# Optimization experiments

Hardware: AMD Instinct MI355X
Metric: run time of the kernel (lower is better)

## Reference

```python
import jax, jax.numpy as jnp
import numpy as np

N_DRUGS = 4096; N_GENE = 5414; N_KG = N_DRUGS + N_GENE
N_MOL = 131072; E_MOL = 524288; E_KG = 524288; R = 8
MLP_IN = 1024; MLP_H = 512; D = 256; GCN_IN = 64; GCN_H = 128
DIM1 = 256; DIM2 = 128; DIM3 = 64; NCLS = 2
EPS = 1e-5


def setup_inputs() -> dict:
    key = jax.random.key(0)
    ks = jax.random.split(key, 32)
    def n(i, shape, fan):
        return jax.random.normal(ks[i], shape, dtype=jnp.float32) * (1.0 / np.sqrt(fan))
    inp = {}
    inp['fp_data'] = jax.random.normal(ks[0], (N_DRUGS, MLP_IN), dtype=jnp.float32)
    inp['mol_x'] = jax.random.normal(ks[1], (N_MOL, GCN_IN), dtype=jnp.float32)
    inp['mol_batch'] = jnp.sort(jax.random.randint(ks[2], (N_MOL,), 0, N_DRUGS))
    inp['mol_edge_index'] = jax.random.randint(ks[3], (2, E_MOL), 0, N_MOL)
    inp['kg_edge_index'] = jax.random.randint(ks[4], (2, E_KG), 0, N_KG)
    inp['kg_edge_type'] = jax.random.randint(ks[5], (E_KG,), 0, R)
    # parameters
    inp['fp_w1'] = n(6, (MLP_IN, MLP_H), MLP_IN); inp['fp_b1'] = jnp.zeros((MLP_H,), jnp.float32)
    inp['fp_w2'] = n(7, (MLP_H, D), MLP_H);       inp['fp_b2'] = jnp.zeros((D,), jnp.float32)
    inp['gcn_w1'] = n(8, (GCN_IN, GCN_H), GCN_IN); inp['gcn_b1'] = jnp.zeros((GCN_H,), jnp.float32)
    inp['gcn_w2'] = n(9, (GCN_H, D), GCN_H);       inp['gcn_b2'] = jnp.zeros((D,), jnp.float32)
    inp['att_w1'] = n(10, (D, 128), D); inp['att_b1'] = jnp.zeros((128,), jnp.float32)
    inp['att_w2'] = n(11, (128,), 128)
    inp['gene_emb'] = jax.random.normal(ks[12], (N_GENE, D), dtype=jnp.float32)
    inp['rg_w1'] = n(13, (R, D, DIM1), D); inp['rg_root1'] = n(14, (D, DIM1), D); inp['rg_b1'] = jnp.zeros((DIM1,), jnp.float32)
    inp['rg_w2'] = n(15, (R, DIM1, DIM2), DIM1); inp['rg_root2'] = n(16, (DIM1, DIM2), DIM1); inp['rg_b2'] = jnp.zeros((DIM2,), jnp.float32)
    inp['lin1_w'] = n(17, (DIM2, DIM3), DIM2); inp['lin1_b'] = jnp.zeros((DIM3,), jnp.float32)
    inp['lin2_w'] = n(18, (DIM3, NCLS), DIM3); inp['lin2_b'] = jnp.zeros((NCLS,), jnp.float32)
    return inp


def bn(x):
    # BatchNorm1d with batch statistics (gamma=1, beta=0)
    m = jnp.mean(x, axis=0, keepdims=True)
    v = jnp.var(x, axis=0, keepdims=True)
    return (x - m) * jax.lax.rsqrt(v + EPS)


def gcn_conv(x, w, b, src, dst, num_nodes):
    # PyG GCNConv: self-loops + symmetric normalization
    loop = jnp.arange(num_nodes, dtype=src.dtype)
    src = jnp.concatenate([src, loop]); dst = jnp.concatenate([dst, loop])
    h = x @ w  # [N, F]
    deg = jnp.zeros((num_nodes,), x.dtype).at[dst].add(1.0)
    dinv = jax.lax.rsqrt(jnp.maximum(deg, 1.0))
    norm = dinv[src] * dinv[dst]  # [E]
    out = jnp.zeros_like(h).at[dst].add(h[src] * norm[:, None])
    return out + b


def rgcn_conv(x, w, root, b, src, dst, etype, num_nodes):
    # PyG RGCNConv (aggr='mean' per relation): out_i = x_i @ root + b + sum_r mean_{j in N_r(i)} x_j @ W_r
    h = jnp.einsum('nd,rdf->rnf', x, w)          # [R, N, F]
    msg = h[etype, src]                          # [E, F] gather by (relation, source)
    cnt = jnp.zeros((R, num_nodes), x.dtype).at[etype, dst].add(1.0)
    norm = 1.0 / jnp.maximum(cnt[etype, dst], 1.0)  # [E]
    agg = jnp.zeros((num_nodes, w.shape[-1]), x.dtype).at[dst].add(msg * norm[:, None])
    return agg + x @ root + b


def forward(fp_data, mol_x, mol_batch, mol_edge_index, kg_edge_index, kg_edge_type,
            fp_w1, fp_b1, fp_w2, fp_b2, gcn_w1, gcn_b1, gcn_w2, gcn_b2,
            att_w1, att_b1, att_w2, gene_emb,
            rg_w1, rg_root1, rg_b1, rg_w2, rg_root2, rg_b2,
            lin1_w, lin1_b, lin2_w, lin2_b):
    # fingerprint MLP branch
    fp = jax.nn.relu(bn(fp_data @ fp_w1 + fp_b1))
    fp = jax.nn.relu(bn(fp @ fp_w2 + fp_b2))      # [N_DRUGS, D]
    # molecular GCN branch (batched graph replaces the dataloader loop)
    msrc, mdst = mol_edge_index[0], mol_edge_index[1]
    g = jax.nn.relu(bn(gcn_conv(mol_x, gcn_w1, gcn_b1, msrc, mdst, N_MOL)))
    g = jax.nn.relu(bn(gcn_conv(g, gcn_w2, gcn_b2, msrc, mdst, N_MOL)))  # [N_MOL, D]
    # global mean pool per molecule
    gsum = jnp.zeros((N_DRUGS, D), g.dtype).at[mol_batch].add(g)
    gcnt = jnp.zeros((N_DRUGS,), g.dtype).at[mol_batch].add(1.0)
    graph_out = gsum / jnp.maximum(gcnt, 1.0)[:, None]  # [N_DRUGS, D]
    # attention fusion of the two views
    z = jnp.stack([graph_out, fp], axis=1)        # [N_DRUGS, 2, D]
    w = jnp.tanh(z @ att_w1 + att_b1) @ att_w2    # [N_DRUGS, 2]
    beta = jax.nn.softmax(w, axis=1)
    emb = jnp.sum(beta[:, :, None] * z, axis=1)   # [N_DRUGS, D]
    # knowledge graph RGCN over drugs + genes
    x = jnp.concatenate([emb, gene_emb], axis=0)  # [N_KG, D]
    ksrc, kdst = kg_edge_index[0], kg_edge_index[1]
    x = jax.nn.relu(bn(rgcn_conv(x, rg_w1, rg_root1, rg_b1, ksrc, kdst, kg_edge_type, N_KG)))
    x = jax.nn.relu(bn(rgcn_conv(x, rg_w2, rg_root2, rg_b2, ksrc, kdst, kg_edge_type, N_KG)))
    x = jax.nn.relu(bn(x @ lin1_w + lin1_b))
    x = x @ lin2_w + lin2_b
    return jax.nn.log_softmax(x, axis=-1), beta[:, :, None]


def reference(fp_data, mol_x, mol_batch, mol_edge_index, kg_edge_index, kg_edge_type,
              fp_w1, fp_b1, fp_w2, fp_b2, gcn_w1, gcn_b1, gcn_w2, gcn_b2,
              att_w1, att_b1, att_w2, gene_emb,
              rg_w1, rg_root1, rg_b1, rg_w2, rg_root2, rg_b2,
              lin1_w, lin1_b, lin2_w, lin2_b):
    return forward(fp_data, mol_x, mol_batch, mol_edge_index, kg_edge_index, kg_edge_type,
                   fp_w1, fp_b1, fp_w2, fp_b2, gcn_w1, gcn_b1, gcn_w2, gcn_b2,
                   att_w1, att_b1, att_w2, gene_emb,
                   rg_w1, rg_root1, rg_b1, rg_w2, rg_root2, rg_b2,
                   lin1_w, lin1_b, lin2_w, lin2_b)
```

## Files before the change

kernel.cpp:

```cpp
#include <hip/hip_runtime.h>
#include <hip/hip_bf16.h>
#include <cstdint>

typedef __hip_bfloat16 bf16;
typedef unsigned short u16;
typedef unsigned int u32;
typedef __attribute__((ext_vector_type(8))) short short8;
typedef __attribute__((ext_vector_type(4))) float f32x4;

__device__ __forceinline__ float tofloat(float x){ return x; }
__device__ __forceinline__ float tofloat(bf16 x){ return __bfloat162float(x); }
__device__ __forceinline__ float b2f(u16 a){ return __uint_as_float(((unsigned)a) << 16); }
__device__ __forceinline__ u16 f2b(float f){
    unsigned u = __float_as_uint(f);
    return (u16)((u + 0x7FFFu + ((u >> 16) & 1u)) >> 16);
}

static inline int divup(long a, long b){ return (int)((a + b - 1) / b); }

#define NBLK_STATS 256

__global__ void zero_int(int* p){ *p = 0; }

__global__ void detect_f32(const u16* __restrict__ h, long n, int* flag)
{
    long i = (long)blockIdx.x * blockDim.x + threadIdx.x;
    long st = (long)gridDim.x * blockDim.x;
    int c = 0;
    for (; i < n; i += st)
        if (((h[i] >> 7) & 0xFF) == 0xFF) c++;
    if (c) atomicAdd(flag, c);
}

struct ConvTab { const void* src[14]; float* dst[14]; u16* dstB[14]; int n[14]; };

__global__ void conv_all(ConvTab t, const int* __restrict__ flagp)
{
    bool f32 = (*flagp != 0);
    int seg = blockIdx.y;
    const void* s = t.src[seg];
    float* d = t.dst[seg];
    u16*   dB = t.dstB[seg];
    int n = t.n[seg];
    long i = (long)blockIdx.x * blockDim.x + threadIdx.x;
    long st = (long)gridDim.x * blockDim.x;
    for (; i < n; i += st) {
        float v = f32 ? ((const float*)s)[i] : tofloat(((const bf16*)s)[i]);
        d[i] = v; dB[i] = f2b(v);
    }
}

__global__ void conv_dual_b16(const void* __restrict__ src, u16* __restrict__ dst,
                              long n, const int* __restrict__ flagp)
{
    bool f32 = (*flagp != 0);
    long i = (long)blockIdx.x * blockDim.x + threadIdx.x;
    long st = (long)gridDim.x * blockDim.x;
    for (; i < n; i += st)
        dst[i] = f32 ? f2b(((const float*)src)[i]) : ((const u16*)src)[i];
}

__global__ void conv_molx(const float* __restrict__ src, u16* __restrict__ dst,
                          long n4, const int* __restrict__ flagp)
{
    if (*flagp == 0) return;
    long i = (long)blockIdx.x * blockDim.x + threadIdx.x;
    long st = (long)gridDim.x * blockDim.x;
    for (; i < n4; i += st) {
        float4 v = ((const float4*)src)[i];
        ushort4 o;
        o.x = f2b(v.x); o.y = f2b(v.y); o.z = f2b(v.z); o.w = f2b(v.w);
        ((ushort4*)dst)[i] = o;
    }
}

struct TransTab { const u16* src[6]; u16* dst[6]; int K[6]; int N[6]; };

__global__ __launch_bounds__(256)
void transpose6(TransTab t)
{
    int s = blockIdx.z;
    int K = t.K[s], N = t.N[s];
    int k0 = blockIdx.x * 32, n0 = blockIdx.y * 32;
    if (k0 >= K || n0 >= N) return;
    const u16* src = t.src[s];
    u16* dst = t.dst[s];
    __shared__ u16 tl[32][33];
    int x = threadIdx.x & 31, y = threadIdx.x >> 5;
    for (int yy = y; yy < 32; yy += 8) {
        int k = k0 + yy, n = n0 + x;
        tl[yy][x] = (k < K && n < N) ? src[(long)k * N + n] : (u16)0;
    }
    __syncthreads();
    for (int yy = y; yy < 32; yy += 8) {
        int n = n0 + yy, k = k0 + x;
        if (n < N && k < K) dst[(long)n * K + k] = tl[x][yy];
    }
}

struct KV3 { const int* key[3]; int* h[3]; long n[3]; };

__global__ void hist3(KV3 t)
{
    int s = blockIdx.y;
    const int* key = t.key[s]; int* h = t.h[s]; long n = t.n[s];
    long i = (long)blockIdx.x * blockDim.x + threadIdx.x;
    long st = (long)gridDim.x * blockDim.x;
    for (; i < n; i += st) atomicAdd(&h[key[i]], 1);
}

struct Scan3 { const int* in[3]; int* out[3]; int* bt[3]; int* bo[3]; int n[3]; };

__global__ __launch_bounds__(1024)
void scan_bsum3(Scan3 t)
{
    int s = blockIdx.y;
    int n = t.n[s];
    int nb = (n + 4095) >> 12;
    if ((int)blockIdx.x >= nb) return;
    const int* in = t.in[s];
    __shared__ int sh[1024];
    int tid = threadIdx.x;
    int i0 = blockIdx.x * 4096 + tid * 4;
    int acc = 0;
#pragma unroll
    for (int k = 0; k < 4; k++) { int idx = i0 + k; acc += (idx < n) ? in[idx] : 0; }
    sh[tid] = acc;
    __syncthreads();
    for (int off = 512; off > 0; off >>= 1) {
        if (tid < off) sh[tid] += sh[tid + off];
        __syncthreads();
    }
    if (tid == 0) t.bt[s][blockIdx.x] = sh[0];
}

__global__ void scan_tiny3(Scan3 t)
{
    int s = blockIdx.x;
    if (threadIdx.x != 0) return;
    int nb = (t.n[s] + 4095) >> 12;
    const int* bt = t.bt[s]; int* bo = t.bo[s];
    int c = 0;
    for (int b = 0; b < nb; b++) { bo[b] = c; c += bt[b]; }
    bo[nb] = c;
}

__global__ __launch_bounds__(1024)
void scan_final3(Scan3 t)
{
    int s = blockIdx.y;
    int n = t.n[s];
    int nb = (n + 4095) >> 12;
    if ((int)blockIdx.x >= nb) return;
    const int* in = t.in[s]; int* out = t.out[s]; const int* bo = t.bo[s];
    __shared__ int buf[1024];
    int tid = threadIdx.x;
    int i0 = blockIdx.x * 4096 + tid * 4;
    int v[4]; int acc = 0;
#pragma unroll
    for (int k = 0; k < 4; k++) {
        int idx = i0 + k;
        v[k] = (idx < n) ? in[idx] : 0;
        acc += v[k];
    }
    buf[tid] = acc;
    __syncthreads();
    for (int off = 1; off < 1024; off <<= 1) {
        int tv = (tid >= off) ? buf[tid - off] : 0;
        __syncthreads();
        buf[tid] += tv;
        __syncthreads();
    }
    int excl = buf[tid] - acc + bo[blockIdx.x];
#pragma unroll
    for (int k = 0; k < 4; k++) {
        int idx = i0 + k;
        if (idx < n) out[idx] = excl;
        excl += v[k];
    }
    if (blockIdx.x == 0 && tid == 0) out[n] = bo[nb];
}

struct Bin3 { const int* key[3]; const int* off[3]; int* cur[3]; int* bins[3]; long n[3]; };

__global__ void bin3(Bin3 t)
{
    int s = blockIdx.y;
    const int* key = t.key[s]; const int* off = t.off[s];
    int* cur = t.cur[s]; int* bins = t.bins[s]; long n = t.n[s];
    long i = (long)blockIdx.x * blockDim.x + threadIdx.x;
    long st = (long)gridDim.x * blockDim.x;
    for (; i < n; i += st) {
        int k = key[i];
        int pos = off[k] + atomicAdd(&cur[k], 1);
        bins[pos] = (int)i;
    }
}

__global__ void kg_key2(const int* __restrict__ dst, const int* __restrict__ et,
                        long E, int* __restrict__ key)
{
    long i = (long)blockIdx.x * blockDim.x + threadIdx.x;
    long st = (long)gridDim.x * blockDim.x;
    for (; i < E; i += st) key[i] = dst[i] * 8 + et[i];
}

__global__ void flatten2(const int* __restrict__ mbins, const int* __restrict__ msrc,
                         const int* __restrict__ mdst, const float* __restrict__ dinv,
                         int2* __restrict__ ebM,
                         const int* __restrict__ kbins, const int* __restrict__ ksrc,
                         int* __restrict__ ebK, long E)
{
    long i = (long)blockIdx.x * blockDim.x + threadIdx.x;
    long st = (long)gridDim.x * blockDim.x;
    if (blockIdx.y == 0) {
        for (; i < E; i += st) {
            int e = mbins[i];
            int sn = msrc[e];
            ebM[i] = make_int2(sn, __float_as_int(dinv[sn] * dinv[mdst[e]]));
        }
    } else {
        for (; i < E; i += st) ebK[i] = ksrc[kbins[i]];
    }
}

__global__ void filli(int* p, long n, int v)
{
    long i = (long)blockIdx.x * blockDim.x + threadIdx.x;
    long st = (long)gridDim.x * blockDim.x;
    for (; i < n; i += st) p[i] = v;
}

__global__ void dinv_from_deg(const int* __restrict__ deg, float* __restrict__ dinv, long n)
{
    long i = (long)blockIdx.x * blockDim.x + threadIdx.x;
    long st = (long)gridDim.x * blockDim.x;
    for (; i < n; i += st) dinv[i] = rsqrtf((float)(deg[i] + 1));
}

template<typename TC, int NBLK, bool STATS>
__global__ __launch_bounds__(256)
void gemm_bt(const u16* __restrict__ A, int lda,
             const u16* __restrict__ BT, int ldbt,
             TC* __restrict__ C, int ldc,
             int M, int N, int K,
             float* __restrict__ SP1, float* __restrict__ SP2, int Ntot)
{
    __shared__ __align__(16) u16 As[64][40];
    __shared__ __align__(16) u16 Bs[NBLK * 64][40];
    __shared__ float st1[NBLK * 64], st2[NBLK * 64];
    const int tid = threadIdx.x;
    const int lane = tid & 63, wave = tid >> 6;
    const int l15 = lane & 15, quad = lane >> 4;
    const int wm = (wave & 1) * 32, wn = (wave >> 1) * 32;
    const int row0 = blockIdx.x * 64, col0 = blockIdx.y * (NBLK * 64);
    const int arow = tid >> 2, ak = (tid & 3) * 8;
    const int aok = row0 + arow < M;

    if (STATS && tid < NBLK * 64) { st1[tid] = 0.f; st2[tid] = 0.f; }

    f32x4 acc[NBLK][2][2];
#pragma unroll
    for (int t = 0; t < NBLK; t++)
#pragma unroll
        for (int i = 0; i < 2; i++)
#pragma unroll
            for (int j = 0; j < 2; j++)
#pragma unroll
                for (int r = 0; r < 4; r++) acc[t][i][j][r] = 0.f;

    const u16* pa = A + (long)(row0 + arow) * lda + ak;
    const u16* pb[NBLK];
#pragma unroll
    for (int t = 0; t < NBLK; t++)
        pb[t] = BT + (long)(col0 + t * 64 + arow) * ldbt + ak;

    ushort4 ra0 = {0,0,0,0}, ra1 = {0,0,0,0};
    ushort4 rb0[NBLK], rb1[NBLK];
    if (aok) { ra0 = *(const ushort4*)pa; ra1 = *(const ushort4*)(pa + 4); }
#pragma unroll
    for (int t = 0; t < NBLK; t++) {
        rb0[t] = *(const ushort4*)pb[t];
        rb1[t] = *(const ushort4*)(pb[t] + 4);
    }

    for (int k0 = 0; k0 < K; k0 += 32) {
        *(ushort4*)&As[arow][ak]     = ra0;
        *(ushort4*)&As[arow][ak + 4] = ra1;
#pragma unroll
        for (int t = 0; t < NBLK; t++) {
            *(ushort4*)&Bs[t * 64 + arow][ak]     = rb0[t];
            *(ushort4*)&Bs[t * 64 + arow][ak + 4] = rb1[t];
        }
        __syncthreads();
        if (k0 + 32 < K) {
            if (aok) {
                ra0 = *(const ushort4*)(pa + k0 + 32);
                ra1 = *(const ushort4*)(pa + k0 + 36);
            }
#pragma unroll
            for (int t = 0; t < NBLK; t++) {
                rb0[t] = *(const ushort4*)(pb[t] + k0 + 32);
                rb1[t] = *(const ushort4*)(pb[t] + k0 + 36);
            }
        }
        short8 a0 = *(const short8*)&As[wm + l15][quad * 8];
        short8 a1 = *(const short8*)&As[wm + 16 + l15][quad * 8];
#pragma unroll
        for (int t = 0; t < NBLK; t++) {
            short8 b0 = *(const short8*)&Bs[t * 64 + wn + l15][quad * 8];
            short8 b1 = *(const short8*)&Bs[t * 64 + wn + 16 + l15][quad * 8];
            acc[t][0][0] = __builtin_amdgcn_mfma_f32_16x16x32_bf16(a0, b0, acc[t][0][0], 0, 0, 0);
            acc[t][0][1] = __builtin_amdgcn_mfma_f32_16x16x32_bf16(a0, b1, acc[t][0][1], 0, 0, 0);
            acc[t][1][0] = __builtin_amdgcn_mfma_f32_16x16x32_bf16(a1, b0, acc[t][1][0], 0, 0, 0);
            acc[t][1][1] = __builtin_amdgcn_mfma_f32_16x16x32_bf16(a1, b1, acc[t][1][1], 0, 0, 0);
        }
        __syncthreads();
    }
#pragma unroll
    for (int t = 0; t < NBLK; t++)
#pragma unroll
        for (int j = 0; j < 2; j++) {
            float s = 0.f, q = 0.f;
#pragma unroll
            for (int i = 0; i < 2; i++)
#pragma unroll
                for (int r = 0; r < 4; r++) {
                    int row = row0 + wm + i * 16 + quad * 4 + r;
                    int col = col0 + t * 64 + wn + j * 16 + l15;
                    float v = acc[t][i][j][r];
                    float y;
                    if constexpr (sizeof(TC) == 2) {
                        u16 h = f2b(v);
                        if (row < M) ((u16*)C)[(long)row * ldc + col] = h;
                        y = b2f(h);
                    } else {
                        if (row < M) ((float*)C)[(long)row * ldc + col] = v;
                        y = v;
                    }
                    if (STATS) { s += y; q += y * y; }
                }
            if (STATS) {
                s += __shfl_xor(s, 16); s += __shfl_xor(s, 32);
                q += __shfl_xor(q, 16); q += __shfl_xor(q, 32);
                if (quad == 0) {
                    atomicAdd(&st1[t * 64 + wn + j * 16 + l15], s);
                    atomicAdd(&st2[t * 64 + wn + j * 16 + l15], q);
                }
            }
        }
    if (STATS) {
        __syncthreads();
        if (tid < NBLK * 64) {
            long off = (long)blockIdx.x * Ntot + (long)blockIdx.y * (NBLK * 64) + tid;
            SP1[off] = st1[tid];
            SP2[off] = st2[tid];
        }
    }
}

__global__ __launch_bounds__(256)
void gemm64(const float* __restrict__ A, int lda,
            const float* __restrict__ B, int ldb,
            float* __restrict__ C, int ldc,
            int M, int N, int K)
{
    __shared__ float As[16][68];
    __shared__ float Bs[16][68];
    const int tid = threadIdx.x;
    const int row0 = blockIdx.x * 64, col0 = blockIdx.y * 64;
    float acc[4][4];
#pragma unroll
    for (int i = 0; i < 4; i++)
#pragma unroll
        for (int j = 0; j < 4; j++) acc[i][j] = 0.f;
    const int ar = tid >> 2, ak = (tid & 3) * 4;
    const int bk = tid >> 4, bc = (tid & 15) * 4;
    const int ty4 = (tid >> 4) * 4, tx4 = (tid & 15) * 4;
    for (int k0 = 0; k0 < K; k0 += 16) {
        {
            int row = row0 + ar;
            float4 v = make_float4(0.f, 0.f, 0.f, 0.f);
            if (row < M) v = *(const float4*)(A + (long)row * lda + k0 + ak);
            As[ak + 0][ar] = v.x; As[ak + 1][ar] = v.y;
            As[ak + 2][ar] = v.z; As[ak + 3][ar] = v.w;
        }
        {
            int c = col0 + bc;
            float4 v = make_float4(0.f, 0.f, 0.f, 0.f);
            if (c < N) v = *(const float4*)(B + (long)(k0 + bk) * ldb + c);
            *(float4*)&Bs[bk][bc] = v;
        }
        __syncthreads();
#pragma unroll
        for (int k = 0; k < 16; k++) {
            float4 a = *(const float4*)&As[k][ty4];
            float4 b = *(const float4*)&Bs[k][tx4];
            acc[0][0] += a.x * b.x; acc[0][1] += a.x * b.y; acc[0][2] += a.x * b.z; acc[0][3] += a.x * b.w;
            acc[1][0] += a.y * b.x; acc[1][1] += a.y * b.y; acc[1][2] += a.y * b.z; acc[1][3] += a.y * b.w;
            acc[2][0] += a.z * b.x; acc[2][1] += a.z * b.y; acc[2][2] += a.z * b.z; acc[2][3] += a.z * b.w;
            acc[3][0] += a.w * b.x; acc[3][1] += a.w * b.y; acc[3][2] += a.w * b.z; acc[3][3] += a.w * b.w;
        }
        __syncthreads();
    }
    int c = col0 + tx4;
#pragma unroll
    for (int i = 0; i < 4; i++) {
        int r = row0 + ty4 + i;
        if (r < M && c < N)
            *(float4*)&C[(long)r * ldc + c] =
                make_float4(acc[i][0], acc[i][1], acc[i][2], acc[i][3]);
    }
}

__global__ __launch_bounds__(256)
void colstats_f32_v2(const float* __restrict__ X, int M, int N,
                     float* __restrict__ p1, float* __restrict__ p2)
{
    __shared__ float sh1[1024], sh2[1024];
    int tid = threadIdx.x;
    int ncg = N >> 2;
    int cg  = tid & (ncg - 1);
    int rg  = tid / ncg;
    int nrg = 256 / ncg;
    float s0=0,s1=0,s2=0,s3=0, q0=0,q1=0,q2=0,q3=0;
    const float* base = X + 4 * cg;
    for (long row = (long)blockIdx.x * nrg + rg; row < M; row += (long)gridDim.x * nrg) {
        float4 v = *(const float4*)(base + row * (long)N);
        s0 += v.x; q0 += v.x * v.x; s1 += v.y; q1 += v.y * v.y;
        s2 += v.z; q2 += v.z * v.z; s3 += v.w; q3 += v.w * v.w;
    }
    float4* S1 = (float4*)sh1; float4* S2 = (float4*)sh2;
    S1[tid] = make_float4(s0, s1, s2, s3);
    S2[tid] = make_float4(q0, q1, q2, q3);
    __syncthreads();
    for (int off = nrg >> 1; off > 0; off >>= 1) {
        if (rg < off) {
            float4 a = S1[tid], b = S1[tid + off * ncg];
            S1[tid] = make_float4(a.x + b.x, a.y + b.y, a.z + b.z, a.w + b.w);
            float4 c = S2[tid], d = S2[tid + off * ncg];
            S2[tid] = make_float4(c.x + d.x, c.y + d.y, c.z + d.z, c.w + d.w);
        }
        __syncthreads();
    }
    if (rg == 0) {
        *(float4*)&p1[(long)blockIdx.x * N + 4 * cg] = S1[tid];
        *(float4*)&p2[(long)blockIdx.x * N + 4 * cg] = S2[tid];
    }
}

__global__ __launch_bounds__(1024)
void colstats_reduce_v3(const float* __restrict__ p1, const float* __restrict__ p2,
                        int nblk, int N, float invM,
                        float* __restrict__ s1o, float* __restrict__ s2o)
{
    __shared__ float sh1[1024], sh2[1024];
    int tid = threadIdx.x;
    int col = blockIdx.x * 64 + (tid & 63);
    int seg = tid >> 6;
    float a = 0.f, c = 0.f;
    for (int b = seg; b < nblk; b += 16) {
        a += p1[(long)b * N + col];
        c += p2[(long)b * N + col];
    }
    sh1[tid] = a; sh2[tid] = c;
    __syncthreads();
    for (int off = 8; off > 0; off >>= 1) {
        if (seg < off) {
            sh1[tid] += sh1[tid + off * 64];
            sh2[tid] += sh2[tid + off * 64];
        }
        __syncthreads();
    }
    if (seg == 0) {
        float mean = sh1[tid] * invM;
        float var  = fmaxf(sh2[tid] * invM - mean * mean, 0.f);
        s1o[col] = mean;
        s2o[col] = rsqrtf(var + 1e-5f);
    }
}

__global__ void bn_apply(float* X, long total, int mask,
                         const float* __restrict__ s1, const float* __restrict__ s2)
{
    long i = (long)blockIdx.x * blockDim.x + threadIdx.x;
    long st = (long)gridDim.x * blockDim.x;
    for (; i < total; i += st) {
        int j = (int)(i & mask);
        X[i] = fmaxf((X[i] - s1[j]) * s2[j], 0.f);
    }
}

__global__ void bn_apply_b16v(u32* __restrict__ X, long n2, int maskHalf,
                              const float* __restrict__ s1, const float* __restrict__ s2)
{
    long i = (long)blockIdx.x * blockDim.x + threadIdx.x;
    long st = (long)gridDim.x * blockDim.x;
    for (; i < n2; i += st) {
        u32 v = X[i];
        int f = (int)(i & maskHalf) * 2;
        float y0 = fmaxf((b2f((u16)(v & 0xFFFF)) - s1[f])     * s2[f],     0.f);
        float y1 = fmaxf((b2f((u16)(v >> 16))    - s1[f + 1]) * s2[f + 1], 0.f);
        X[i] = (u32)f2b(y0) | ((u32)f2b(y1) << 16);
    }
}

__global__ __launch_bounds__(256)
void mol_agg_in(const void* __restrict__ Xraw, const u16* __restrict__ Xcvt,
                const int* __restrict__ flagp, const float* __restrict__ dinv,
                const int* __restrict__ off, const int2* __restrict__ eb,
                int NM, u16* __restrict__ out)
{
    const u16* X = (*flagp != 0) ? Xcvt : (const u16*)Xraw;
    int wid  = (int)(((long)blockIdx.x * 256 + threadIdx.x) >> 6);
    int lane = threadIdx.x & 63;
    if (wid >= NM) return;
    float dv = dinv[wid];
    float acc = b2f(X[(long)wid * 64 + lane]) * dv * dv;
    int j = off[wid], j1 = off[wid + 1];
    for (; j + 3 < j1; j += 4) {
        int2 e0 = eb[j], e1 = eb[j + 1], e2 = eb[j + 2], e3 = eb[j + 3];
        float v0 = b2f(X[(long)e0.x * 64 + lane]);
        float v1 = b2f(X[(long)e1.x * 64 + lane]);
        float v2 = b2f(X[(long)e2.x * 64 + lane]);
        float v3 = b2f(X[(long)e3.x * 64 + lane]);
        acc += v0 * __int_as_float(e0.y) + v1 * __int_as_float(e1.y)
             + v2 * __int_as_float(e2.y) + v3 * __int_as_float(e3.y);
    }
    for (; j < j1; j++) {
        int2 e = eb[j];
        acc += b2f(X[(long)e.x * 64 + lane]) * __int_as_float(e.y);
    }
    out[(long)wid * 64 + lane] = f2b(acc);
}

__global__ __launch_bounds__(256)
void mol_agg128_bn(const u16* __restrict__ G, const float* __restrict__ dinv,
                   const int* __restrict__ off, const int2* __restrict__ eb,
                   int NM, const float* __restrict__ s1, const float* __restrict__ s2,
                   u16* __restrict__ out)
{
    int wid  = (int)(((long)blockIdx.x * 256 + threadIdx.x) >> 6);
    int lane = threadIdx.x & 63;
    if (wid >= NM) return;
    const float m0 = s1[2 * lane],     r0 = s2[2 * lane];
    const float m1 = s1[2 * lane + 1], r1 = s2[2 * lane + 1];
    float dv = dinv[wid], dv2 = dv * dv;
    u32 u = *(const u32*)(G + (long)wid * 128 + 2 * lane);
    float a0 = fmaxf((b2f((u16)(u & 0xFFFF)) - m0) * r0, 0.f) * dv2;
    float a1 = fmaxf((b2f((u16)(u >> 16))    - m1) * r1, 0.f) * dv2;
    int j = off[wid], j1 = off[wid + 1];
    for (; j + 3 < j1; j += 4) {
        int2 e0 = eb[j], e1 = eb[j + 1], e2 = eb[j + 2], e3 = eb[j + 3];
        u32 v0 = *(const u32*)(G + (long)e0.x * 128 + 2 * lane);
        u32 v1 = *(const u32*)(G + (long)e1.x * 128 + 2 * lane);
        u32 v2 = *(const u32*)(G + (long)e2.x * 128 + 2 * lane);
        u32 v3 = *(const u32*)(G + (long)e3.x * 128 + 2 * lane);
        float n0 = __int_as_float(e0.y), n1 = __int_as_float(e1.y);
        float n2 = __int_as_float(e2.y), n3 = __int_as_float(e3.y);
        a0 += fmaxf((b2f((u16)(v0 & 0xFFFF)) - m0) * r0, 0.f) * n0
            + fmaxf((b2f((u16)(v1 & 0xFFFF)) - m0) * r0, 0.f) * n1
            + fmaxf((b2f((u16)(v2 & 0xFFFF)) - m0) * r0, 0.f) * n2
            + fmaxf((b2f((u16)(v3 & 0xFFFF)) - m0) * r0, 0.f) * n3;
        a1 += fmaxf((b2f((u16)(v0 >> 16)) - m1) * r1, 0.f) * n0
            + fmaxf((b2f((u16)(v1 >> 16)) - m1) * r1, 0.f) * n1
            + fmaxf((b2f((u16)(v2 >> 16)) - m1) * r1, 0.f) * n2
            + fmaxf((b2f((u16)(v3 >> 16)) - m1) * r1, 0.f) * n3;
    }
    for (; j < j1; j++) {
        int2 e = eb[j];
        u32 v = *(const u32*)(G + (long)e.x * 128 + 2 * lane);
        float n = __int_as_float(e.y);
        a0 += fmaxf((b2f((u16)(v & 0xFFFF)) - m0) * r0, 0.f) * n;
        a1 += fmaxf((b2f((u16)(v >> 16))    - m1) * r1, 0.f) * n;
    }
    u32 o = (u32)f2b(a0) | ((u32)f2b(a1) << 16);
    *(u32*)(out + (long)wid * 128 + 2 * lane) = o;
}

__global__ __launch_bounds__(256)
void kg_preagg2(const u16* __restrict__ xin, const int* __restrict__ off2,
                const int* __restrict__ eb, int NSEG, int NKG, u16* __restrict__ aggx)
{
    int seg  = (int)(((long)blockIdx.x * 256 + threadIdx.x) >> 6);
    int lane = threadIdx.x & 63;
    const int c4 = 4 * lane;
    if (seg >= NSEG + NKG) return;
    if (seg >= NSEG) {
        int node = seg - NSEG;
        *(ushort4*)(aggx + (long)node * 2304 + c4) =
            *(const ushort4*)(xin + (long)node * 256 + c4);
        return;
    }
    int node = seg >> 3, r = seg & 7;
    int j0 = off2[seg], j1 = off2[seg + 1];
    float a0 = 0.f, a1 = 0.f, a2 = 0.f, a3 = 0.f;
    int j = j0;
    for (; j + 3 < j1; j += 4) {
        int s0 = eb[j], s1 = eb[j + 1], s2 = eb[j + 2], s3 = eb[j + 3];
        ushort4 v0 = *(const ushort4*)(xin + (long)s0 * 256 + c4);
        ushort4 v1 = *(const ushort4*)(xin + (long)s1 * 256 + c4);
        ushort4 v2 = *(const ushort4*)(xin + (long)s2 * 256 + c4);
        ushort4 v3 = *(const ushort4*)(xin + (long)s3 * 256 + c4);
        a0 += b2f(v0.x) + b2f(v1.x) + b2f(v2.x) + b2f(v3.x);
        a1 += b2f(v0.y) + b2f(v1.y) + b2f(v2.y) + b2f(v3.y);
        a2 += b2f(v0.z) + b2f(v1.z) + b2f(v2.z) + b2f(v3.z);
        a3 += b2f(v0.w) + b2f(v1.w) + b2f(v2.w) + b2f(v3.w);
    }
    for (; j < j1; j++) {
        ushort4 v = *(const ushort4*)(xin + (long)eb[j] * 256 + c4);
        a0 += b2f(v.x); a1 += b2f(v.y); a2 += b2f(v.z); a3 += b2f(v.w);
    }
    float nrm = 1.0f / fmaxf((float)(j1 - j0), 1.0f);
    ushort4 o;
    o.x = f2b(a0 * nrm); o.y = f2b(a1 * nrm);
    o.z = f2b(a2 * nrm); o.w = f2b(a3 * nrm);
    *(ushort4*)(aggx + (long)node * 2304 + 256 + (r << 8) + c4) = o;
}

__global__ __launch_bounds__(256)
void pool128(const u16* __restrict__ g, const int* __restrict__ off,
             const int* __restrict__ bins, int ND,
             const float* __restrict__ s1, const float* __restrict__ s2,
             float* __restrict__ gout, int c0out)
{
    int wid  = (int)(((long)blockIdx.x * 256 + threadIdx.x) >> 6);
    int lane = threadIdx.x & 63;
    if (wid >= ND) return;
    const float m0 = s1[2 * lane],     r0 = s2[2 * lane];
    const float m1 = s1[2 * lane + 1], r1 = s2[2 * lane + 1];
    int j0 = off[wid], j1 = off[wid + 1];
    float a0 = 0.f, a1 = 0.f;
    for (int j = j0; j < j1; j++) {
        u32 v = *(const u32*)(g + (long)bins[j] * 128 + 2 * lane);
        a0 += fmaxf((b2f((u16)(v & 0xFFFF)) - m0) * r0, 0.f);
        a1 += fmaxf((b2f((u16)(v >> 16))    - m1) * r1, 0.f);
    }
    float inv = 1.0f / fmaxf((float)(j1 - j0), 1.0f);
    *(float2*)(gout + (long)wid * 256 + c0out + 2 * lane) =
        make_float2(a0 * inv, a1 * inv);
}

__global__ void attention_fuse(const float* __restrict__ go, const float* __restrict__ fpv,
                               const float* __restrict__ fs1, const float* __restrict__ fs2,
                               const float* __restrict__ W1, const float* __restrict__ B1,
                               const float* __restrict__ W2,
                               u16* __restrict__ embb, float* __restrict__ beta_out)
{
    int d = blockIdx.x;
    int t = threadIdx.x;
    __shared__ float z[2][256];
    __shared__ float red[128];
    for (int c = t; c < 256; c += 128) {
        z[0][c] = go[(long)d * 256 + c];
        z[1][c] = fmaxf((fpv[(long)d * 256 + c] - fs1[c]) * fs2[c], 0.f);
    }
    __syncthreads();
    float s[2];
    for (int v = 0; v < 2; v++) {
        float acc = B1[t];
        for (int k = 0; k < 256; k++) acc += z[v][k] * W1[k * 128 + t];
        red[t] = tanhf(acc) * W2[t];
        __syncthreads();
        for (int off = 64; off > 0; off >>= 1) {
            if (t < off) red[t] += red[t + off];
            __syncthreads();
        }
        s[v] = red[0];
        __syncthreads();
    }
    float m = fmaxf(s[0], s[1]);
    float e0 = expf(s[0] - m), e1 = expf(s[1] - m);
    float inv = 1.0f / (e0 + e1);
    float b0 = e0 * inv, b1 = e1 * inv;
    for (int c = t; c < 256; c += 128)
        embb[(long)d * 256 + c] = f2b(b0 * z[0][c] + b1 * z[1][c]);
    if (t == 0) {
        beta_out[d * 2 + 0] = b0;
        beta_out[d * 2 + 1] = b1;
    }
}

__global__ void logits_out_bn(const float* __restrict__ x4,
                              const float* __restrict__ s1, const float* __restrict__ s2,
                              const float* __restrict__ w, const float* __restrict__ b,
                              float* __restrict__ out, int NKG)
{
    int i = blockIdx.x * blockDim.x + threadIdx.x;
    if (i >= NKG) return;
    float a0 = b[0], a1 = b[1];
    for (int k = 0; k < 64; k++) {
        float v = fmaxf((x4[(long)i * 64 + k] - s1[k]) * s2[k], 0.f);
        a0 += v * w[k * 2 + 0];
        a1 += v * w[k * 2 + 1];
    }
    float m = fmaxf(a0, a1);
    float lse = m + logf(expf(a0 - m) + expf(a1 - m));
    out[i * 2 + 0] = a0 - lse;
    out[i * 2 + 1] = a1 - lse;
}

extern "C" void kernel_launch(void* const* d_in, const int* in_sizes, int n_in,
                              void* d_out, int out_size, void* d_ws, size_t ws_size,
                              hipStream_t stream)
{
    (void)in_sizes; (void)n_in; (void)out_size; (void)ws_size;
    const int ND = 4096, NM = 131072, NKG = 9510, NGENE = 5414;
    const long EM = 524288, EK = 524288;
    const int NSEG = 8 * NKG;

    const void* fp_data = d_in[0];
    const void* mol_x   = d_in[1];
    const int*  mol_batch = (const int*)d_in[2];
    const int*  mol_ei  = (const int*)d_in[3];
    const int*  kg_ei   = (const int*)d_in[4];
    const int*  kg_et   = (const int*)d_in[5];

    const int* mol_src = mol_ei;
    const int* mol_dst = mol_ei + EM;
    const int* kg_src  = kg_ei;
    const int* kg_dst  = kg_ei + EK;

    float* out_ls   = (float*)d_out;
    float* out_beta = (float*)d_out + 19020;

    char* wp = (char*)d_ws;
    auto carve = [&](size_t bytes) { char* p = wp; wp += (bytes + 255) & ~(size_t)255; return p; };
    float* stats   = (float*)carve(4096);
    float* statsFP = (float*)carve(4096);
    int*   flag  = (int*)carve(256);
    float* dinv  = (float*)carve((size_t)NM * 4);
    float* part1 = (float*)carve((size_t)2048 * 128 * 4);
    float* part2 = (float*)carve((size_t)2048 * 128 * 4);
    int*   sbt3  = (int*)carve(3 * 64 * 4);
    int*   sbo3  = (int*)carve(3 * 64 * 4);
    float* Wpool = (float*)carve((size_t)1630000 * 4);
    u16*   WpoolB= (u16*)carve((size_t)1630000 * 2);
    u16*   WpoolT= (u16*)carve((size_t)1600000 * 2);
    float* fpb   = (float*)carve((size_t)ND * 256 * 4);
    float* gout  = (float*)carve((size_t)ND * 256 * 4);
    int*   key2  = (int*)carve((size_t)EK * 4);
    int*   koff2 = (int*)carve((size_t)(NSEG + 1) * 4);
    char*  z0    = wp;
    int* kdeg2 = (int*)carve((size_t)NSEG * 4);
    int* kcur2 = (int*)carve((size_t)NSEG * 4);
    int* mdeg = (int*)carve((size_t)NM * 4);
    int* mcur = (int*)carve((size_t)NM * 4);
    int* pdeg = (int*)carve((size_t)ND * 4);
    int* pcur = (int*)carve((size_t)ND * 4);
    char*  z1    = wp;
    int* moff = (int*)carve((size_t)(NM + 1) * 4);
    int* mbins= (int*)carve((size_t)EM * 4);
    int* kbins= (int*)carve((size_t)EK * 4);
    int* poff = (int*)carve((size_t)(ND + 1) * 4);
    int* pbins= (int*)carve((size_t)NM * 4);
    char*  REG1  = carve((size_t)NM * 128 * 2);
    char*  REG2  = carve((size_t)NM * 128 * 2);
    u16*   HB    = (u16*)carve((size_t)NM * 64 * 2);

    u16*   XB  = (u16*)REG1;
    u16*   G1  = (u16*)REG1;
    u16*   H2  = (u16*)REG1;
    u16*   x2b = (u16*)REG1;
    float* x3  = (float*)REG1 + (size_t)NKG * 512;
    float* x4  = x3 + (size_t)NKG * 128;
    u16*   xb  = (u16*)(x4 + (size_t)NKG * 64);
    u16*   Xfb = (u16*)REG2;
    u16*   G1A = (u16*)REG2;
    u16*   AGGX= (u16*)REG2;
    u16*   fp1b = HB;
    u16*   Xagg = HB;
    int2* ebM  = (int2*)gout;
    int*  ebK2 = key2;

    zero_int<<<1, 1, 0, stream>>>(flag);
    detect_f32<<<1024, 256, 0, stream>>>((const u16*)fp_data, (long)ND * 1024, flag);
    ConvTab tab;
    const int widx[14] = {6, 8, 10, 12, 14, 15, 16, 19, 18, 22, 21, 24, 26, 27};
    const int wn[14]   = {1024*512, 512*256, 64*128, 128*256, 256*128, 128, 128,
                          256*256, 8*256*256, 256*128, 8*256*128, 128*64, 64*2, 2};
    float* wf[14]; u16* wb[14];
    {
        size_t o = 0;
        for (int i = 0; i < 14; i++) {
            tab.src[i]  = d_in[widx[i]];
            tab.dst[i]  = Wpool + o;
            tab.dstB[i] = WpoolB + o;
            tab.n[i]    = wn[i];
            wf[i] = Wpool + o; wb[i] = WpoolB + o;
            o += (size_t)wn[i];
        }
    }
    conv_all<<<dim3(32, 14), 256, 0, stream>>>(tab, flag);
    float *att_w1c = wf[4], *att_b1c = wf[5], *att_w2c = wf[6];
    float *lin1_wc = wf[11], *lin2_wc = wf[12], *lin2_bc = wf[13];

    u16* T_fpw1  = WpoolT;
    u16* T_fpw2  = T_fpw1 + (size_t)512 * 1024;
    u16* T_gcnw1 = T_fpw2 + (size_t)256 * 512;
    u16* T_gcnw2 = T_gcnw1 + (size_t)128 * 64;
    u16* T_w1    = T_gcnw2 + (size_t)256 * 128;
    u16* T_w2    = T_w1 + (size_t)256 * 2304;
    TransTab tt;
    tt.src[0] = wb[0]; tt.dst[0] = T_fpw1;  tt.K[0] = 1024; tt.N[0] = 512;
    tt.src[1] = wb[1]; tt.dst[1] = T_fpw2;  tt.K[1] = 512;  tt.N[1] = 256;
    tt.src[2] = wb[2]; tt.dst[2] = T_gcnw1; tt.K[2] = 64;   tt.N[2] = 128;
    tt.src[3] = wb[3]; tt.dst[3] = T_gcnw2; tt.K[3] = 128;  tt.N[3] = 256;
    tt.src[4] = wb[7]; tt.dst[4] = T_w1;    tt.K[4] = 2304; tt.N[4] = 256;
    tt.src[5] = wb[9]; tt.dst[5] = T_w2;    tt.K[5] = 2304; tt.N[5] = 128;
    transpose6<<<dim3(72, 16, 6), 256, 0, stream>>>(tt);

    filli<<<512, 256, 0, stream>>>((int*)z0, (long)(z1 - z0) / 4, 0);
    kg_key2<<<2048, 256, 0, stream>>>(kg_dst, kg_et, EK, key2);
    {
        KV3 hv;
        hv.key[0] = mol_dst;   hv.h[0] = mdeg;  hv.n[0] = EM;
        hv.key[1] = key2;      hv.h[1] = kdeg2; hv.n[1] = EK;
        hv.key[2] = mol_batch; hv.h[2] = pdeg;  hv.n[2] = NM;
        hist3<<<dim3(2048, 3), 256, 0, stream>>>(hv);
    }
    dinv_from_deg<<<512, 256, 0, stream>>>(mdeg, dinv, NM);
    {
        Scan3 sc;
        sc.in[0] = mdeg;  sc.out[0] = moff;  sc.n[0] = NM;
        sc.in[1] = kdeg2; sc.out[1] = koff2; sc.n[1] = NSEG;
        sc.in[2] = pdeg;  sc.out[2] = poff;  sc.n[2] = ND;
        for (int s = 0; s < 3; s++) { sc.bt[s] = sbt3 + s * 64; sc.bo[s] = sbo3 + s * 64; }
        scan_bsum3<<<dim3(32, 3), 1024, 0, stream>>>(sc);
        scan_tiny3<<<3, 64, 0, stream>>>(sc);
        scan_final3<<<dim3(32, 3), 1024, 0, stream>>>(sc);
    }
    {
        Bin3 bv;
        bv.key[0] = mol_dst;   bv.off[0] = moff;  bv.cur[0] = mcur;  bv.bins[0] = mbins; bv.n[0] = EM;
        bv.key[1] = key2;      bv.off[1] = koff2; bv.cur[1] = kcur2; bv.bins[1] = kbins; bv.n[1] = EK;
        bv.key[2] = mol_batch; bv.off[2] = poff;  bv.cur[2] = pcur;  bv.bins[2] = pbins; bv.n[2] = NM;
        bin3<<<dim3(2048, 3), 256, 0, stream>>>(bv);
    }
    flatten2<<<dim3(2048, 2), 256, 0, stream>>>(mbins, mol_src, mol_dst, dinv, ebM,
                                                kbins, kg_src, ebK2, EM);

    auto reduceNto = [&](int nblk, int N, float invM, float* s1o, float* s2o) {
        colstats_reduce_v3<<<N / 64, 1024, 0, stream>>>(part1, part2, nblk, N,
                                                        invM, s1o, s2o);
    };

    conv_dual_b16<<<2048, 256, 0, stream>>>(fp_data, Xfb, (long)ND * 1024, flag);
    gemm_bt<u16, 2, true><<<dim3(64, 4), 256, 0, stream>>>(
        Xfb, 1024, T_fpw1, 1024, fp1b, 512, ND, 512, 1024, part1, part2, 512);
    reduceNto(64, 512, 1.0f / ND, stats, stats + 512);
    bn_apply_b16v<<<2048, 256, 0, stream>>>((u32*)fp1b, (long)ND * 256, 255,
                                            stats, stats + 512);
    gemm_bt<float, 1, true><<<dim3(64, 4), 256, 0, stream>>>(
        fp1b, 512, T_fpw2, 512, fpb, 256, ND, 256, 512, part1, part2, 256);
    reduceNto(64, 256, 1.0f / ND, statsFP, statsFP + 512);

    conv_molx<<<2048, 256, 0, stream>>>((const float*)mol_x, XB, (long)NM * 16, flag);
    mol_agg_in<<<32768, 256, 0, stream>>>(mol_x, XB, flag, dinv, moff, ebM, NM, Xagg);
    gemm_bt<u16, 2, true><<<dim3(2048, 1), 256, 0, stream>>>(
        Xagg, 64, T_gcnw1, 64, G1, 128, NM, 128, 64, part1, part2, 128);
    reduceNto(2048, 128, 1.0f / NM, stats, stats + 512);

    mol_agg128_bn<<<32768, 256, 0, stream>>>(G1, dinv, moff, ebM, NM,
                                             stats, stats + 512, G1A);
    for (int h = 0; h < 2; h++) {
        gemm_bt<u16, 2, true><<<dim3(2048, 1), 256, 0, stream>>>(
            G1A, 128, T_gcnw2 + (size_t)h * 128 * 128, 128, H2, 128, NM, 128, 128,
            part1, part2, 128);
        reduceNto(2048, 128, 1.0f / NM, stats, stats + 512);
        pool128<<<1024, 256, 0, stream>>>(H2, poff, pbins, ND,
                                          stats, stats + 512, gout, h * 128);
    }

    attention_fuse<<<ND, 128, 0, stream>>>(gout, fpb, statsFP, statsFP + 512,
                                           att_w1c, att_b1c, att_w2c,
                                           xb, out_beta);
    conv_dual_b16<<<512, 256, 0, stream>>>(d_in[17], xb + (long)ND * 256,
                                           (long)NGENE * 256, flag);

    kg_preagg2<<<divup((long)(NSEG + NKG) * 64, 256), 256, 0, stream>>>(
        xb, koff2, ebK2, NSEG, NKG, AGGX);
    gemm_bt<u16, 2, true><<<dim3(divup(NKG, 64), 2), 256, 0, stream>>>(
        AGGX, 2304, T_w1, 2304, x2b, 256, NKG, 256, 2304, part1, part2, 256);
    reduceNto(divup(NKG, 64), 256, 1.0f / NKG, stats, stats + 512);
    bn_apply_b16v<<<1024, 256, 0, stream>>>((u32*)x2b, (long)NKG * 128, 127,
                                            stats, stats + 512);

    kg_preagg2<<<divup((long)(NSEG + NKG) * 64, 256), 256, 0, stream>>>(
        x2b, koff2, ebK2, NSEG, NKG, AGGX);
    gemm_bt<float, 1, true><<<dim3(divup(NKG, 64), 2), 256, 0, stream>>>(
        AGGX, 2304, T_w2, 2304, x3, 128, NKG, 128, 2304, part1, part2, 128);
    reduceNto(divup(NKG, 64), 128, 1.0f / NKG, stats, stats + 512);
    bn_apply<<<2048, 256, 0, stream>>>(x3, (long)NKG * 128, 127, stats, stats + 512);

    gemm64<<<dim3(divup(NKG, 64), 1, 1), 256, 0, stream>>>(
        x3, 128, lin1_wc, 64, x4, 64, NKG, 64, 128);
    colstats_f32_v2<<<NBLK_STATS, 256, 0, stream>>>(x4, NKG, 64, part1, part2);
    reduceNto(NBLK_STATS, 64, 1.0f / NKG, stats, stats + 512);
    logits_out_bn<<<divup(NKG, 256), 256, 0, stream>>>(x4, stats, stats + 512,
                                                       lin2_wc, lin2_bc, out_ls, NKG);
}
```

Baseline: 986.6 us.

## Scatter edges directly into CSR slots and binary-search sorted pooling offsets

The binning kernel now writes each edge's final payload straight into its CSR slot: source index plus normalisation weight for the molecule graph, and source node for the KG. This removes the separate bins arrays and the flatten pass with its indirect gathers. Pooling offsets are now found by binary search over the sorted batch vector instead of a histogram, scan and bin pass, so pooling reads node rows contiguously. The change relies on mol_batch being sorted, and ebK2 gets its own buffer because it can no longer alias key2.

```diff
diff --git a/kernel.cpp b/kernel.cpp
--- a/kernel.cpp
+++ b/kernel.cpp
@@ -98,9 +98,9 @@
     }
 }
 
-struct KV3 { const int* key[3]; int* h[3]; long n[3]; };
-
-__global__ void hist3(KV3 t)
+struct KV2 { const int* key[2]; int* h[2]; long n[2]; };
+
+__global__ void hist2(KV2 t)
 {
     int s = blockIdx.y;
     const int* key = t.key[s]; int* h = t.h[s]; long n = t.n[s];
@@ -109,10 +109,10 @@
     for (; i < n; i += st) atomicAdd(&h[key[i]], 1);
 }
 
-struct Scan3 { const int* in[3]; int* out[3]; int* bt[3]; int* bo[3]; int n[3]; };
+struct Scan2 { const int* in[2]; int* out[2]; int* bt[2]; int* bo[2]; int n[2]; };
 
 __global__ __launch_bounds__(1024)
-void scan_bsum3(Scan3 t)
+void scan_bsum2(Scan2 t)
 {
     int s = blockIdx.y;
     int n = t.n[s];
@@ -134,7 +134,7 @@
     if (tid == 0) t.bt[s][blockIdx.x] = sh[0];
 }
 
-__global__ void scan_tiny3(Scan3 t)
+__global__ void scan_tiny2(Scan2 t)
 {
     int s = blockIdx.x;
     if (threadIdx.x != 0) return;
@@ -146,7 +146,7 @@
 }
 
 __global__ __launch_bounds__(1024)
-void scan_final3(Scan3 t)
+void scan_final2(Scan2 t)
 {
     int s = blockIdx.y;
     int n = t.n[s];
@@ -181,19 +181,27 @@
     if (blockIdx.x == 0 && tid == 0) out[n] = bo[nb];
 }
 
-struct Bin3 { const int* key[3]; const int* off[3]; int* cur[3]; int* bins[3]; long n[3]; };
-
-__global__ void bin3(Bin3 t)
-{
-    int s = blockIdx.y;
-    const int* key = t.key[s]; const int* off = t.off[s];
-    int* cur = t.cur[s]; int* bins = t.bins[s]; long n = t.n[s];
-    long i = (long)blockIdx.x * blockDim.x + threadIdx.x;
-    long st = (long)gridDim.x * blockDim.x;
-    for (; i < n; i += st) {
-        int k = key[i];
-        int pos = off[k] + atomicAdd(&cur[k], 1);
-        bins[pos] = (int)i;
+__global__ void bin_direct(const int* __restrict__ mdst, const int* __restrict__ msrc,
+                           const int* __restrict__ moff, int* __restrict__ mcur,
+                           const float* __restrict__ dinv, int2* __restrict__ ebM,
+                           const int* __restrict__ kkey, const int* __restrict__ ksrc,
+                           const int* __restrict__ koff, int* __restrict__ kcur,
+                           int* __restrict__ ebK, long E)
+{
+    long i = (long)blockIdx.x * blockDim.x + threadIdx.x;
+    long st = (long)gridDim.x * blockDim.x;
+    if (blockIdx.y == 0) {
+        for (; i < E; i += st) {
+            int d = mdst[i], sn = msrc[i];
+            int pos = moff[d] + atomicAdd(&mcur[d], 1);
+            ebM[pos] = make_int2(sn, __float_as_int(dinv[sn] * dinv[d]));
+        }
+    } else {
+        for (; i < E; i += st) {
+            int k = kkey[i];
+            int pos = koff[k] + atomicAdd(&kcur[k], 1);
+            ebK[pos] = ksrc[i];
+        }
     }
 }
 
@@ -205,23 +213,14 @@
     for (; i < E; i += st) key[i] = dst[i] * 8 + et[i];
 }
 
-__global__ void flatten2(const int* __restrict__ mbins, const int* __restrict__ msrc,
-                         const int* __restrict__ mdst, const float* __restrict__ dinv,
-                         int2* __restrict__ ebM,
-                         const int* __restrict__ kbins, const int* __restrict__ ksrc,
-                         int* __restrict__ ebK, long E)
-{
-    long i = (long)blockIdx.x * blockDim.x + threadIdx.x;
-    long st = (long)gridDim.x * blockDim.x;
-    if (blockIdx.y == 0) {
-        for (; i < E; i += st) {
-            int e = mbins[i];
-            int sn = msrc[e];
-            ebM[i] = make_int2(sn, __float_as_int(dinv[sn] * dinv[mdst[e]]));
-        }
-    } else {
-        for (; i < E; i += st) ebK[i] = ksrc[kbins[i]];
-    }
+__global__ void poff_bsearch(const int* __restrict__ batch, int NMn, int NDn,
+                             int* __restrict__ poff)
+{
+    int d = blockIdx.x * blockDim.x + threadIdx.x;
+    if (d > NDn) return;
+    int lo = 0, hi = NMn;
+    while (lo < hi) { int mid = (lo + hi) >> 1; if (batch[mid] < d) lo = mid + 1; else hi = mid; }
+    poff[d] = lo;
 }
 
 __global__ void filli(int* p, long n, int v)
@@ -619,8 +618,7 @@
 }
 
 __global__ __launch_bounds__(256)
-void pool128(const u16* __restrict__ g, const int* __restrict__ off,
-             const int* __restrict__ bins, int ND,
+void pool128(const u16* __restrict__ g, const int* __restrict__ off, int ND,
              const float* __restrict__ s1, const float* __restrict__ s2,
              float* __restrict__ gout, int c0out)
 {
@@ -632,7 +630,7 @@
     int j0 = off[wid], j1 = off[wid + 1];
     float a0 = 0.f, a1 = 0.f;
     for (int j = j0; j < j1; j++) {
-        u32 v = *(const u32*)(g + (long)bins[j] * 128 + 2 * lane);
+        u32 v = *(const u32*)(g + (long)j * 128 + 2 * lane);
         a0 += fmaxf((b2f((u16)(v & 0xFFFF)) - m0) * r0, 0.f);
         a1 += fmaxf((b2f((u16)(v >> 16))    - m1) * r1, 0.f);
     }
@@ -732,8 +730,8 @@
     float* dinv  = (float*)carve((size_t)NM * 4);
     float* part1 = (float*)carve((size_t)2048 * 128 * 4);
     float* part2 = (float*)carve((size_t)2048 * 128 * 4);
-    int*   sbt3  = (int*)carve(3 * 64 * 4);
-    int*   sbo3  = (int*)carve(3 * 64 * 4);
+    int*   sbt2  = (int*)carve(2 * 64 * 4);
+    int*   sbo2  = (int*)carve(2 * 64 * 4);
     float* Wpool = (float*)carve((size_t)1630000 * 4);
     u16*   WpoolB= (u16*)carve((size_t)1630000 * 2);
     u16*   WpoolT= (u16*)carve((size_t)1600000 * 2);
@@ -741,19 +739,15 @@
     float* gout  = (float*)carve((size_t)ND * 256 * 4);
     int*   key2  = (int*)carve((size_t)EK * 4);
     int*   koff2 = (int*)carve((size_t)(NSEG + 1) * 4);
+    int*   ebK2  = (int*)carve((size_t)EK * 4);
+    int*   poff  = (int*)carve((size_t)(ND + 1) * 4);
     char*  z0    = wp;
     int* kdeg2 = (int*)carve((size_t)NSEG * 4);
     int* kcur2 = (int*)carve((size_t)NSEG * 4);
     int* mdeg = (int*)carve((size_t)NM * 4);
     int* mcur = (int*)carve((size_t)NM * 4);
-    int* pdeg = (int*)carve((size_t)ND * 4);
-    int* pcur = (int*)carve((size_t)ND * 4);
     char*  z1    = wp;
     int* moff = (int*)carve((size_t)(NM + 1) * 4);
-    int* mbins= (int*)carve((size_t)EM * 4);
-    int* kbins= (int*)carve((size_t)EK * 4);
-    int* poff = (int*)carve((size_t)(ND + 1) * 4);
-    int* pbins= (int*)carve((size_t)NM * 4);
     char*  REG1  = carve((size_t)NM * 128 * 2);
     char*  REG2  = carve((size_t)NM * 128 * 2);
     u16*   HB    = (u16*)carve((size_t)NM * 64 * 2);
@@ -771,7 +765,6 @@
     u16*   fp1b = HB;
     u16*   Xagg = HB;
     int2* ebM  = (int2*)gout;
-    int*  ebK2 = key2;
 
     zero_int<<<1, 1, 0, stream>>>(flag);
     detect_f32<<<1024, 256, 0, stream>>>((const u16*)fp_data, (long)ND * 1024, flag);
@@ -813,32 +806,26 @@
     filli<<<512, 256, 0, stream>>>((int*)z0, (long)(z1 - z0) / 4, 0);
     kg_key2<<<2048, 256, 0, stream>>>(kg_dst, kg_et, EK, key2);
     {
-        KV3 hv;
-        hv.key[0] = mol_dst;   hv.h[0] = mdeg;  hv.n[0] = EM;
-        hv.key[1] = key2;      hv.h[1] = kdeg2; hv.n[1] = EK;
-        hv.key[2] = mol_batch; hv.h[2] = pdeg;  hv.n[2] = NM;
-        hist3<<<dim3(2048, 3), 256, 0, stream>>>(hv);
+        KV2 hv;
+        hv.key[0] = mol_dst; hv.h[0] = mdeg;  hv.n[0] = EM;
+        hv.key[1] = key2;    hv.h[1] = kdeg2; hv.n[1] = EK;
+        hist2<<<dim3(2048, 2), 256, 0, stream>>>(hv);
     }
     dinv_from_deg<<<512, 256, 0, stream>>>(mdeg, dinv, NM);
+    poff_bsearch<<<divup(ND + 1, 256), 256, 0, stream>>>(mol_batch, NM, ND, poff);
     {
-        Scan3 sc;
+        Scan2 sc;
         sc.in[0] = mdeg;  sc.out[0] = moff;  sc.n[0] = NM;
         sc.in[1] = kdeg2; sc.out[1] = koff2; sc.n[1] = NSEG;
-        sc.in[2] = pdeg;  sc.out[2] = poff;  sc.n[2] = ND;
-        for (int s = 0; s < 3; s++) { sc.bt[s] = sbt3 + s * 64; sc.bo[s] = sbo3 + s * 64; }
-        scan_bsum3<<<dim3(32, 3), 1024, 0, stream>>>(sc);
-        scan_tiny3<<<3, 64, 0, stream>>>(sc);
-        scan_final3<<<dim3(32, 3), 1024, 0, stream>>>(sc);
-    }
-    {
-        Bin3 bv;
-        bv.key[0] = mol_dst;   bv.off[0] = moff;  bv.cur[0] = mcur;  bv.bins[0] = mbins; bv.n[0] = EM;
-        bv.key[1] = key2;      bv.off[1] = koff2; bv.cur[1] = kcur2; bv.bins[1] = kbins; bv.n[1] = EK;
-        bv.key[2] = mol_batch; bv.off[2] = poff;  bv.cur[2] = pcur;  bv.bins[2] = pbins; bv.n[2] = NM;
-        bin3<<<dim3(2048, 3), 256, 0, stream>>>(bv);
-    }
-    flatten2<<<dim3(2048, 2), 256, 0, stream>>>(mbins, mol_src, mol_dst, dinv, ebM,
-                                                kbins, kg_src, ebK2, EM);
+        for (int s = 0; s < 2; s++) { sc.bt[s] = sbt2 + s * 64; sc.bo[s] = sbo2 + s * 64; }
+        scan_bsum2<<<dim3(32, 2), 1024, 0, stream>>>(sc);
+        scan_tiny2<<<2, 64, 0, stream>>>(sc);
+        scan_final2<<<dim3(32, 2), 1024, 0, stream>>>(sc);
+    }
+    bin_direct<<<dim3(2048, 2), 256, 0, stream>>>(mol_dst, mol_src, moff, mcur,
+                                                  dinv, ebM,
+                                                  key2, kg_src, koff2, kcur2,
+                                                  ebK2, EM);
 
     auto reduceNto = [&](int nblk, int N, float invM, float* s1o, float* s2o) {
         colstats_reduce_v3<<<N / 64, 1024, 0, stream>>>(part1, part2, nblk, N,
@@ -868,7 +855,7 @@
             G1A, 128, T_gcnw2 + (size_t)h * 128 * 128, 128, H2, 128, NM, 128, 128,
             part1, part2, 128);
         reduceNto(2048, 128, 1.0f / NM, stats, stats + 512);
-        pool128<<<1024, 256, 0, stream>>>(H2, poff, pbins, ND,
+        pool128<<<1024, 256, 0, stream>>>(H2, poff, ND,
                                           stats, stats + 512, gout, h * 128);
     }
 
```

Measured after the change: 918.2 us. 1.07x faster.
